# Kernel tuning notes

Hardware: AMD Instinct MI355X
Metric: run time of the kernel (lower is better)

The kernel has to match this reference:

```python
import jax, jax.numpy as jnp
import numpy as np

N_NODES = 50000
N_EDGES = 800000
D_IN = 128
D_OUT = 128


def setup_inputs() -> dict:
    key = jax.random.key(0)
    k1, k2, k3 = jax.random.split(key, 3)
    x = jax.random.normal(k1, (N_NODES, D_IN), dtype=jnp.float32)
    edge_index = jax.random.randint(k2, (2, N_EDGES), 0, N_NODES, dtype=jnp.int64)
    # glorot init for weight, zeros for bias
    limit = float(np.sqrt(6.0 / (D_IN + D_OUT)))
    W = jax.random.uniform(k3, (D_IN, D_OUT), dtype=jnp.float32, minval=-limit, maxval=limit)
    b = jnp.zeros((D_OUT,), dtype=jnp.float32)
    return {"x": x, "edge_index": edge_index, "W": W, "b": b}


def reference(x, edge_index, W, b):
    # GCNConv forward: dense transform, then sym-normalized propagation with self-loops.
    N = x.shape[0]
    h = x @ W  # [N, D_OUT]

    src = edge_index[0]
    dst = edge_index[1]
    # add self loops (fill weight = 1.0 since improved=False)
    loop = jnp.arange(N, dtype=src.dtype)
    src = jnp.concatenate([src, loop])
    dst = jnp.concatenate([dst, loop])
    ew = jnp.ones(src.shape[0], dtype=h.dtype)

    # sym normalization: D^{-1/2} A D^{-1/2}
    deg = jax.ops.segment_sum(ew, dst, num_segments=N)  # [N]
    deg_inv_sqrt = jnp.where(deg > 0, jax.lax.rsqrt(jnp.maximum(deg, 1e-12)), 0.0)
    norm = deg_inv_sqrt[src] * ew * deg_inv_sqrt[dst]  # [E+N]

    # message = norm * x_j ; aggregate = scatter-add to dst
    msg = norm[:, None] * h[src]  # [E+N, D_OUT]
    out = jax.ops.segment_sum(msg, dst, num_segments=N)  # [N, D_OUT]
    return out + b
```

## Files before the change

kernel.cpp:

```cpp
#include <hip/hip_runtime.h>
#include <math.h>

#define N_NODES 50000
#define N_EDGES 800000
#define D 128
#define NBKT 392
#define CHUNK 4096
#define NCHUNK ((N_EDGES + CHUNK - 1) / CHUNK)
#define CAPB 4096

typedef short bf16x8 __attribute__((ext_vector_type(8)));
typedef float f32x4 __attribute__((ext_vector_type(4)));

static __device__ __forceinline__ unsigned short f2bf_rn(float f) {
    unsigned u = __float_as_uint(f);
    unsigned r = (u + 0x7FFF + ((u >> 16) & 1)) >> 16;
    return (unsigned short)r;
}
static __device__ __forceinline__ float bf2f(unsigned short h) {
    return __uint_as_float(((unsigned)h) << 16);
}


__global__ __launch_bounds__(256) void compress_hist(const int* __restrict__ ei,
                                                     unsigned short* __restrict__ s16,
                                                     unsigned short* __restrict__ d16,
                                                     int* __restrict__ bcnt) {
    __shared__ int lh[NBKT];
    int t = threadIdx.x;
    for (int j = t; j < NBKT; j += 256) lh[j] = 0;
    __syncthreads();
    for (int e = blockIdx.x * 256 + t; e < N_EDGES; e += gridDim.x * 256) {
        int s = ei[e];
        int d = ei[N_EDGES + e];
        s16[e] = (unsigned short)s;
        d16[e] = (unsigned short)d;
        atomicAdd(&lh[d >> 7], 1);
    }
    __syncthreads();
    for (int j = t; j < NBKT; j += 256) {
        int c = lh[j];
        if (c) atomicAdd(&bcnt[j], c);
    }
}


__global__ __launch_bounds__(256) void bscan(const int* __restrict__ bcnt,
                                             int* __restrict__ bbase,
                                             int* __restrict__ gcur,
                                             int* __restrict__ row_start) {
    __shared__ int sm[256];
    int t = threadIdx.x;
    int i0 = 2 * t, i1 = i0 + 1;
    int a = (i0 < NBKT) ? bcnt[i0] : 0;
    int b = (i1 < NBKT) ? bcnt[i1] : 0;
    int ps = a + b;
    sm[t] = ps; __syncthreads();
    for (int o = 1; o < 256; o <<= 1) {
        int ad = (t >= o) ? sm[t - o] : 0;
        __syncthreads();
        sm[t] += ad;
        __syncthreads();
    }
    int ex = sm[t] - ps;
    if (i0 < NBKT) { bbase[i0] = ex;     gcur[i0] = i0 * CAPB; }
    if (i1 < NBKT) { bbase[i1] = ex + a; gcur[i1] = i1 * CAPB; }
    if (t == 0) row_start[N_NODES] = N_EDGES;
}


__global__ __launch_bounds__(256) void partition(const unsigned short* __restrict__ s16,
                                                 const unsigned short* __restrict__ d16,
                                                 int* __restrict__ gcur,
                                                 unsigned int* __restrict__ part) {
    __shared__ unsigned int ebuf[CHUNK];
    __shared__ unsigned int obuf[CHUNK];
    __shared__ int hist[NBKT];
    __shared__ int spos[NBKT];
    __shared__ int goff[NBKT];
    __shared__ int sm[256];
    int t = threadIdx.x;
    int base = blockIdx.x * CHUNK;
    int n = N_EDGES - base; if (n > CHUNK) n = CHUNK;

    for (int j = t; j < NBKT; j += 256) hist[j] = 0;
    __syncthreads();
    for (int i = t; i < n; i += 256) {
        unsigned s = s16[base + i];
        unsigned d = d16[base + i];
        ebuf[i] = s | (d << 16);
        atomicAdd(&hist[d >> 7], 1);
    }
    __syncthreads();
    int i0 = 2 * t, i1 = i0 + 1;
    int a = (i0 < NBKT) ? hist[i0] : 0;
    int b = (i1 < NBKT) ? hist[i1] : 0;
    int ps = a + b;
    sm[t] = ps; __syncthreads();
    for (int o = 1; o < 256; o <<= 1) {
        int ad = (t >= o) ? sm[t - o] : 0;
        __syncthreads();
        sm[t] += ad;
        __syncthreads();
    }
    int ex = sm[t] - ps;
    if (i0 < NBKT) spos[i0] = ex;
    if (i1 < NBKT) spos[i1] = ex + a;
    __syncthreads();
    for (int j = t; j < NBKT; j += 256) {
        int gp = atomicAdd(&gcur[j], hist[j]);
        goff[j] = gp - spos[j];
    }
    __syncthreads();
    for (int j = t; j < NBKT; j += 256) hist[j] = 0;
    __syncthreads();
    for (int i = t; i < n; i += 256) {
        unsigned e = ebuf[i];
        int bk = e >> 23;
        int p = spos[bk] + atomicAdd(&hist[bk], 1);
        obuf[p] = e;
    }
    __syncthreads();
    for (int i = t; i < n; i += 256) {
        unsigned e = obuf[i];
        int bk = e >> 23;
        part[goff[bk] + i] = e;
    }
}


__global__ __launch_bounds__(256) void csr_build(const unsigned int* __restrict__ part,
                                                 const int* __restrict__ bcnt,
                                                 const int* __restrict__ bbase,
                                                 int* __restrict__ row_start,
                                                 float* __restrict__ dinv,
                                                 unsigned short* __restrict__ ssrc16) {
    __shared__ unsigned int ebuf[CAPB];
    __shared__ unsigned short img[CAPB];
    __shared__ int h128[128];
    __shared__ int loff[128];
    __shared__ int sm[128];
    int t = threadIdx.x;
    int b = blockIdx.x;
    int cnt = bcnt[b];
    int gb = b * CAPB;
    int cb = bbase[b];
    int nbase = b * 128;

    for (int j = t; j < 128; j += 256) h128[j] = 0;
    __syncthreads();
    for (int i = t; i < cnt; i += 256) {
        unsigned e = part[gb + i];
        ebuf[i] = e;
        atomicAdd(&h128[(e >> 16) & 127], 1);
    }
    __syncthreads();
    if (t < 128) sm[t] = h128[t];
    __syncthreads();
    for (int o = 1; o < 128; o <<= 1) {
        int ad = 0;
        if (t < 128 && t >= o) ad = sm[t - o];
        __syncthreads();
        if (t < 128) sm[t] += ad;
        __syncthreads();
    }
    if (t < 128) {
        int ex = sm[t] - h128[t];
        loff[t] = ex;
        int node = nbase + t;
        if (node < N_NODES) {
            row_start[node] = cb + ex;
            dinv[node] = rsqrtf((float)(h128[t] + 1));
        }
        h128[t] = 0;
    }
    __syncthreads();
    for (int i = t; i < cnt; i += 256) {
        unsigned e = ebuf[i];
        int j = (e >> 16) & 127;
        int p = loff[j] + atomicAdd(&h128[j], 1);
        img[p] = (unsigned short)(e & 0xffffu);
    }
    __syncthreads();
    for (int i = t; i < cnt; i += 256) ssrc16[cb + i] = img[i];
}


__global__ __launch_bounds__(256) void prep_w(const float* __restrict__ W,
                                              unsigned short* __restrict__ wH,
                                              unsigned short* __restrict__ wL) {
    int tid = blockIdx.x * 256 + threadIdx.x;
    if (tid >= 2048) return;
    int kstep = tid >> 9;
    int ct = (tid >> 6) & 7;
    int lane = tid & 63;
    int kbase = kstep * 32 + ((lane >> 4) << 3);
    int c = ct * 16 + (lane & 15);
    #pragma unroll
    for (int e = 0; e < 8; ++e) {
        float v = W[(kbase + e) * 128 + c];
        unsigned short hb = f2bf_rn(v);
        float res = v - bf2f(hb);
        unsigned short lb = f2bf_rn(res);
        wH[tid * 8 + e] = hb;
        wL[tid * 8 + e] = lb;
    }
}


__global__ __launch_bounds__(256) void gemm_xw_mfma(const float* __restrict__ x,
                                                    const unsigned short* __restrict__ wH,
                                                    const unsigned short* __restrict__ wL,
                                                    unsigned short* __restrict__ h) {
    int wave = threadIdx.x >> 6;
    int lane = threadIdx.x & 63;
    int rowbase = blockIdx.x * 64 + wave * 16;

    f32x4 acc[8];
    #pragma unroll
    for (int ct = 0; ct < 8; ++ct) acc[ct] = (f32x4)(0.f);

    int arow = rowbase + (lane & 15);
    if (arow >= N_NODES) arow = N_NODES - 1;
    const float* xrow = x + (size_t)arow * 128 + ((lane >> 4) << 3);

    #pragma unroll
    for (int kstep = 0; kstep < 4; ++kstep) {
        float4 a0 = *(const float4*)(xrow + kstep * 32);
        float4 a1 = *(const float4*)(xrow + kstep * 32 + 4);
        float av[8] = {a0.x, a0.y, a0.z, a0.w, a1.x, a1.y, a1.z, a1.w};
        bf16x8 ah, al;
        #pragma unroll
        for (int e = 0; e < 8; ++e) {
            unsigned short hb = f2bf_rn(av[e]);
            float res = av[e] - bf2f(hb);
            ah[e] = (short)hb;
            al[e] = (short)f2bf_rn(res);
        }
        const bf16x8* bh = (const bf16x8*)(wH + (size_t)(kstep * 8) * 64 * 8 + lane * 8);
        const bf16x8* bl = (const bf16x8*)(wL + (size_t)(kstep * 8) * 64 * 8 + lane * 8);
        #pragma unroll
        for (int ct = 0; ct < 8; ++ct) {
            bf16x8 bhv = bh[ct * 64];
            bf16x8 blv = bl[ct * 64];
            acc[ct] = __builtin_amdgcn_mfma_f32_16x16x32_bf16(ah, bhv, acc[ct], 0, 0, 0);
            acc[ct] = __builtin_amdgcn_mfma_f32_16x16x32_bf16(ah, blv, acc[ct], 0, 0, 0);
            acc[ct] = __builtin_amdgcn_mfma_f32_16x16x32_bf16(al, bhv, acc[ct], 0, 0, 0);
        }
    }

    int rbase = rowbase + ((lane >> 4) << 2);
    int col = lane & 15;
    #pragma unroll
    for (int ct = 0; ct < 8; ++ct) {
        #pragma unroll
        for (int i = 0; i < 4; ++i) {
            int row = rbase + i;
            if (row < N_NODES) h[(size_t)row * 128 + ct * 16 + col] = f2bf_rn(acc[ct][i]);
        }
    }
}


__global__ __launch_bounds__(256) void aggregate(const unsigned int* __restrict__ hu,
                                                 const int* __restrict__ row_start,
                                                 const unsigned short* __restrict__ ssrc16,
                                                 const float* __restrict__ dinv,
                                                 const float* __restrict__ bias,
                                                 float* __restrict__ out) {
    int node = blockIdx.x * 4 + (threadIdx.x >> 6);
    int lane = threadIdx.x & 63;
    if (node >= N_NODES) return;
    int s = row_start[node];
    int t = row_start[node + 1];
    float accx = 0.f, accy = 0.f;
    for (int base = s; base < t; base += 64) {
        int c = t - base;
        if (c > 64) c = 64;
        int li = base + (lane < c ? lane : c - 1);
        int idx = (int)ssrc16[li];
        float dv = dinv[idx];
        int j = 0;
        for (; j + 4 <= c; j += 4) {
            int s0 = __shfl(idx, j), s1 = __shfl(idx, j + 1);
            int s2 = __shfl(idx, j + 2), s3 = __shfl(idx, j + 3);
            float d0 = __shfl(dv, j), d1 = __shfl(dv, j + 1);
            float d2 = __shfl(dv, j + 2), d3 = __shfl(dv, j + 3);
            unsigned u0 = hu[(size_t)s0 * 64 + lane];
            unsigned u1 = hu[(size_t)s1 * 64 + lane];
            unsigned u2 = hu[(size_t)s2 * 64 + lane];
            unsigned u3 = hu[(size_t)s3 * 64 + lane];
            accx += d0 * __uint_as_float(u0 << 16) + d1 * __uint_as_float(u1 << 16)
                  + d2 * __uint_as_float(u2 << 16) + d3 * __uint_as_float(u3 << 16);
            accy += d0 * __uint_as_float(u0 & 0xffff0000u) + d1 * __uint_as_float(u1 & 0xffff0000u)
                  + d2 * __uint_as_float(u2 & 0xffff0000u) + d3 * __uint_as_float(u3 & 0xffff0000u);
        }
        for (; j < c; ++j) {
            int sj = __shfl(idx, j);
            float dj = __shfl(dv, j);
            unsigned u = hu[(size_t)sj * 64 + lane];
            accx += dj * __uint_as_float(u << 16);
            accy += dj * __uint_as_float(u & 0xffff0000u);
        }
    }
    float di = dinv[node];
    unsigned us = hu[(size_t)node * 64 + lane];
    float2 bv = *(const float2*)&bias[2 * lane];
    float2 o;
    o.x = di * accx + di * di * __uint_as_float(us << 16) + bv.x;
    o.y = di * accy + di * di * __uint_as_float(us & 0xffff0000u) + bv.y;
    *(float2*)&out[(size_t)node * 128 + 2 * lane] = o;
}


extern "C" void kernel_launch(void* const* d_in, const int* in_sizes, int n_in,
                              void* d_out, int out_size, void* d_ws, size_t ws_size,
                              hipStream_t stream) {
    const float* x  = (const float*)d_in[0];
    const int*   ei = (const int*)d_in[1];
    const float* W  = (const float*)d_in[2];
    const float* b  = (const float*)d_in[3];
    float* out = (float*)d_out;

    char* ws = (char*)d_ws;
    unsigned short* h      = (unsigned short*)(ws + 0);
    unsigned short* s16    = (unsigned short*)(ws + 0);
    unsigned short* d16    = (unsigned short*)(ws + 1600000);
    unsigned int*   part   = (unsigned int*)  (ws + 3200000);
    int*   row_start       = (int*)  (ws + 12800000);
    float* dinv            = (float*)(ws + 13000016);
    unsigned short* ssrc16 = (unsigned short*)(ws + 13200016);
    int*   bcnt            = (int*)  (ws + 14800016);
    int*   bbase           = (int*)  (ws + 14801600);
    int*   gcur            = (int*)  (ws + 14803200);
    unsigned short* wH     = (unsigned short*)(ws + 14804800);
    unsigned short* wL     = (unsigned short*)(ws + 14837568);

    hipMemsetAsync(bcnt, 0, NBKT * sizeof(int), stream);
    hipLaunchKernelGGL(compress_hist, dim3(256),    dim3(256), 0, stream, ei, s16, d16, bcnt);
    hipLaunchKernelGGL(bscan,         dim3(1),      dim3(256), 0, stream, bcnt, bbase, gcur, row_start);
    hipLaunchKernelGGL(partition,     dim3(NCHUNK), dim3(256), 0, stream, s16, d16, gcur, part);
    hipLaunchKernelGGL(csr_build,     dim3(NBKT),   dim3(256), 0, stream, part, bcnt, bbase, row_start, dinv, ssrc16);
    hipLaunchKernelGGL(prep_w,        dim3(8),      dim3(256), 0, stream, W, wH, wL);
    hipLaunchKernelGGL(gemm_xw_mfma,  dim3((N_NODES + 63) / 64), dim3(256), 0, stream, x, wH, wL, h);
    hipLaunchKernelGGL(aggregate,     dim3((N_NODES + 3) / 4), dim3(256), 0, stream,
                       (const unsigned int*)h, row_start, ssrc16, dinv, b, out);
}
```

Baseline: 163.0 us.

## Drop histogram pre-pass; derive bucket counts from partition cursors

Removes the compress_hist and bscan kernels and the memset. Partition now reads the int edge_index directly and csr_build recomputes the per-bucket prefix sum from the final cursor values, with W prep merged into a single setup kernel. The aim is to cut launches and the extra pass over the edge list. The aggregate gather loop is also widened from 4 to 8 outstanding loads per step to raise memory-level parallelism. Every csr_build block redoes the small scan, and the wider unroll raises register pressure.

```diff
diff --git a/kernel.cpp b/kernel.cpp
--- a/kernel.cpp
+++ b/kernel.cpp
@@ -22,55 +22,34 @@
 }
 
 
-__global__ __launch_bounds__(256) void compress_hist(const int* __restrict__ ei,
-                                                     unsigned short* __restrict__ s16,
-                                                     unsigned short* __restrict__ d16,
-                                                     int* __restrict__ bcnt) {
-    __shared__ int lh[NBKT];
-    int t = threadIdx.x;
-    for (int j = t; j < NBKT; j += 256) lh[j] = 0;
-    __syncthreads();
-    for (int e = blockIdx.x * 256 + t; e < N_EDGES; e += gridDim.x * 256) {
-        int s = ei[e];
-        int d = ei[N_EDGES + e];
-        s16[e] = (unsigned short)s;
-        d16[e] = (unsigned short)d;
-        atomicAdd(&lh[d >> 7], 1);
-    }
-    __syncthreads();
-    for (int j = t; j < NBKT; j += 256) {
-        int c = lh[j];
-        if (c) atomicAdd(&bcnt[j], c);
-    }
-}
-
-
-__global__ __launch_bounds__(256) void bscan(const int* __restrict__ bcnt,
-                                             int* __restrict__ bbase,
+__global__ __launch_bounds__(256) void setup(const float* __restrict__ W,
+                                             unsigned short* __restrict__ wH,
+                                             unsigned short* __restrict__ wL,
                                              int* __restrict__ gcur,
                                              int* __restrict__ row_start) {
-    __shared__ int sm[256];
-    int t = threadIdx.x;
-    int i0 = 2 * t, i1 = i0 + 1;
-    int a = (i0 < NBKT) ? bcnt[i0] : 0;
-    int b = (i1 < NBKT) ? bcnt[i1] : 0;
-    int ps = a + b;
-    sm[t] = ps; __syncthreads();
-    for (int o = 1; o < 256; o <<= 1) {
-        int ad = (t >= o) ? sm[t - o] : 0;
-        __syncthreads();
-        sm[t] += ad;
-        __syncthreads();
-    }
-    int ex = sm[t] - ps;
-    if (i0 < NBKT) { bbase[i0] = ex;     gcur[i0] = i0 * CAPB; }
-    if (i1 < NBKT) { bbase[i1] = ex + a; gcur[i1] = i1 * CAPB; }
-    if (t == 0) row_start[N_NODES] = N_EDGES;
-}
-
-
-__global__ __launch_bounds__(256) void partition(const unsigned short* __restrict__ s16,
-                                                 const unsigned short* __restrict__ d16,
+    if (blockIdx.x < 8) {
+        int tid = blockIdx.x * 256 + threadIdx.x;
+        int kstep = tid >> 9;
+        int ct = (tid >> 6) & 7;
+        int lane = tid & 63;
+        int kbase = kstep * 32 + ((lane >> 4) << 3);
+        int c = ct * 16 + (lane & 15);
+        #pragma unroll
+        for (int e = 0; e < 8; ++e) {
+            float v = W[(kbase + e) * 128 + c];
+            unsigned short hb = f2bf_rn(v);
+            float res = v - bf2f(hb);
+            wH[tid * 8 + e] = hb;
+            wL[tid * 8 + e] = f2bf_rn(res);
+        }
+    } else {
+        for (int j = threadIdx.x; j < NBKT; j += 256) gcur[j] = j * CAPB;
+        if (threadIdx.x == 0) row_start[N_NODES] = N_EDGES;
+    }
+}
+
+
+__global__ __launch_bounds__(256) void partition(const int* __restrict__ ei,
                                                  int* __restrict__ gcur,
                                                  unsigned int* __restrict__ part) {
     __shared__ unsigned int ebuf[CHUNK];
@@ -86,8 +65,8 @@
     for (int j = t; j < NBKT; j += 256) hist[j] = 0;
     __syncthreads();
     for (int i = t; i < n; i += 256) {
-        unsigned s = s16[base + i];
-        unsigned d = d16[base + i];
+        unsigned s = (unsigned)ei[base + i];
+        unsigned d = (unsigned)ei[N_EDGES + base + i];
         ebuf[i] = s | (d << 16);
         atomicAdd(&hist[d >> 7], 1);
     }
@@ -130,25 +109,42 @@
 
 
 __global__ __launch_bounds__(256) void csr_build(const unsigned int* __restrict__ part,
-                                                 const int* __restrict__ bcnt,
-                                                 const int* __restrict__ bbase,
+                                                 const int* __restrict__ gcur,
                                                  int* __restrict__ row_start,
                                                  float* __restrict__ dinv,
                                                  unsigned short* __restrict__ ssrc16) {
     __shared__ unsigned int ebuf[CAPB];
     __shared__ unsigned short img[CAPB];
+    __shared__ int exf[NBKT];
+    __shared__ int sm2[256];
     __shared__ int h128[128];
     __shared__ int loff[128];
     __shared__ int sm[128];
     int t = threadIdx.x;
     int b = blockIdx.x;
-    int cnt = bcnt[b];
+
+    int i0 = 2 * t, i1 = i0 + 1;
+    int a = (i0 < NBKT) ? (gcur[i0] - i0 * CAPB) : 0;
+    int b2 = (i1 < NBKT) ? (gcur[i1] - i1 * CAPB) : 0;
+    int ps = a + b2;
+    sm2[t] = ps; __syncthreads();
+    for (int o = 1; o < 256; o <<= 1) {
+        int ad = (t >= o) ? sm2[t - o] : 0;
+        __syncthreads();
+        sm2[t] += ad;
+        __syncthreads();
+    }
+    int ex = sm2[t] - ps;
+    if (i0 < NBKT) exf[i0] = ex;
+    if (i1 < NBKT) exf[i1] = ex + a;
+    for (int j = t; j < 128; j += 256) h128[j] = 0;
+    __syncthreads();
+
+    int cnt = gcur[b] - b * CAPB;
+    int cb = exf[b];
     int gb = b * CAPB;
-    int cb = bbase[b];
     int nbase = b * 128;
 
-    for (int j = t; j < 128; j += 256) h128[j] = 0;
-    __syncthreads();
     for (int i = t; i < cnt; i += 256) {
         unsigned e = part[gb + i];
         ebuf[i] = e;
@@ -165,11 +161,11 @@
         __syncthreads();
     }
     if (t < 128) {
-        int ex = sm[t] - h128[t];
-        loff[t] = ex;
+        int exl = sm[t] - h128[t];
+        loff[t] = exl;
         int node = nbase + t;
         if (node < N_NODES) {
-            row_start[node] = cb + ex;
+            row_start[node] = cb + exl;
             dinv[node] = rsqrtf((float)(h128[t] + 1));
         }
         h128[t] = 0;
@@ -183,28 +179,6 @@
     }
     __syncthreads();
     for (int i = t; i < cnt; i += 256) ssrc16[cb + i] = img[i];
-}
-
-
-__global__ __launch_bounds__(256) void prep_w(const float* __restrict__ W,
-                                              unsigned short* __restrict__ wH,
-                                              unsigned short* __restrict__ wL) {
-    int tid = blockIdx.x * 256 + threadIdx.x;
-    if (tid >= 2048) return;
-    int kstep = tid >> 9;
-    int ct = (tid >> 6) & 7;
-    int lane = tid & 63;
-    int kbase = kstep * 32 + ((lane >> 4) << 3);
-    int c = ct * 16 + (lane & 15);
-    #pragma unroll
-    for (int e = 0; e < 8; ++e) {
-        float v = W[(kbase + e) * 128 + c];
-        unsigned short hb = f2bf_rn(v);
-        float res = v - bf2f(hb);
-        unsigned short lb = f2bf_rn(res);
-        wH[tid * 8 + e] = hb;
-        wL[tid * 8 + e] = lb;
-    }
 }
 
 
@@ -281,19 +255,20 @@
         int idx = (int)ssrc16[li];
         float dv = dinv[idx];
         int j = 0;
-        for (; j + 4 <= c; j += 4) {
-            int s0 = __shfl(idx, j), s1 = __shfl(idx, j + 1);
-            int s2 = __shfl(idx, j + 2), s3 = __shfl(idx, j + 3);
-            float d0 = __shfl(dv, j), d1 = __shfl(dv, j + 1);
-            float d2 = __shfl(dv, j + 2), d3 = __shfl(dv, j + 3);
-            unsigned u0 = hu[(size_t)s0 * 64 + lane];
-            unsigned u1 = hu[(size_t)s1 * 64 + lane];
-            unsigned u2 = hu[(size_t)s2 * 64 + lane];
-            unsigned u3 = hu[(size_t)s3 * 64 + lane];
-            accx += d0 * __uint_as_float(u0 << 16) + d1 * __uint_as_float(u1 << 16)
-                  + d2 * __uint_as_float(u2 << 16) + d3 * __uint_as_float(u3 << 16);
-            accy += d0 * __uint_as_float(u0 & 0xffff0000u) + d1 * __uint_as_float(u1 & 0xffff0000u)
-                  + d2 * __uint_as_float(u2 & 0xffff0000u) + d3 * __uint_as_float(u3 & 0xffff0000u);
+        for (; j + 8 <= c; j += 8) {
+            int ss[8]; float dd[8]; unsigned uu[8];
+            #pragma unroll
+            for (int k = 0; k < 8; ++k) {
+                ss[k] = __shfl(idx, j + k);
+                dd[k] = __shfl(dv, j + k);
+            }
+            #pragma unroll
+            for (int k = 0; k < 8; ++k) uu[k] = hu[(size_t)ss[k] * 64 + lane];
+            #pragma unroll
+            for (int k = 0; k < 8; ++k) {
+                accx += dd[k] * __uint_as_float(uu[k] << 16);
+                accy += dd[k] * __uint_as_float(uu[k] & 0xffff0000u);
+            }
         }
         for (; j < c; ++j) {
             int sj = __shfl(idx, j);
@@ -324,25 +299,18 @@
 
     char* ws = (char*)d_ws;
     unsigned short* h      = (unsigned short*)(ws + 0);
-    unsigned short* s16    = (unsigned short*)(ws + 0);
-    unsigned short* d16    = (unsigned short*)(ws + 1600000);
-    unsigned int*   part   = (unsigned int*)  (ws + 3200000);
+    unsigned int*   part   = (unsigned int*)  (ws + 0);
     int*   row_start       = (int*)  (ws + 12800000);
     float* dinv            = (float*)(ws + 13000016);
     unsigned short* ssrc16 = (unsigned short*)(ws + 13200016);
-    int*   bcnt            = (int*)  (ws + 14800016);
-    int*   bbase           = (int*)  (ws + 14801600);
-    int*   gcur            = (int*)  (ws + 14803200);
-    unsigned short* wH     = (unsigned short*)(ws + 14804800);
-    unsigned short* wL     = (unsigned short*)(ws + 14837568);
-
-    hipMemsetAsync(bcnt, 0, NBKT * sizeof(int), stream);
-    hipLaunchKernelGGL(compress_hist, dim3(256),    dim3(256), 0, stream, ei, s16, d16, bcnt);
-    hipLaunchKernelGGL(bscan,         dim3(1),      dim3(256), 0, stream, bcnt, bbase, gcur, row_start);
-    hipLaunchKernelGGL(partition,     dim3(NCHUNK), dim3(256), 0, stream, s16, d16, gcur, part);
-    hipLaunchKernelGGL(csr_build,     dim3(NBKT),   dim3(256), 0, stream, part, bcnt, bbase, row_start, dinv, ssrc16);
-    hipLaunchKernelGGL(prep_w,        dim3(8),      dim3(256), 0, stream, W, wH, wL);
-    hipLaunchKernelGGL(gemm_xw_mfma,  dim3((N_NODES + 63) / 64), dim3(256), 0, stream, x, wH, wL, h);
-    hipLaunchKernelGGL(aggregate,     dim3((N_NODES + 3) / 4), dim3(256), 0, stream,
+    int*   gcur            = (int*)  (ws + 14800016);
+    unsigned short* wH     = (unsigned short*)(ws + 14801600);
+    unsigned short* wL     = (unsigned short*)(ws + 14834368);
+
+    hipLaunchKernelGGL(setup,        dim3(9),      dim3(256), 0, stream, W, wH, wL, gcur, row_start);
+    hipLaunchKernelGGL(partition,    dim3(NCHUNK), dim3(256), 0, stream, ei, gcur, part);
+    hipLaunchKernelGGL(csr_build,    dim3(NBKT),   dim3(256), 0, stream, part, gcur, row_start, dinv, ssrc16);
+    hipLaunchKernelGGL(gemm_xw_mfma, dim3((N_NODES + 63) / 64), dim3(256), 0, stream, x, wH, wL, h);
+    hipLaunchKernelGGL(aggregate,    dim3((N_NODES + 3) / 4), dim3(256), 0, stream,
                        (const unsigned int*)h, row_start, ssrc16, dinv, b, out);
 }
```

After: 149.5 us. -8.3%, faster.
